# Optimization experiments

Hardware: AMD Instinct MI355X
Metric: run time of the kernel (lower is better)

Reference implementation:

```python
import jax, jax.numpy as jnp
import numpy as np

D_MODEL = 2048
N_HEADS = 16
D_HEAD = D_MODEL // N_HEADS
D_FF = 4 * D_MODEL
LN_EPS = 1e-5


def setup_inputs() -> dict:
    key = jax.random.key(0)
    ks = jax.random.split(key, 12)
    s = 1.0 / np.sqrt(D_MODEL)
    sf = 1.0 / np.sqrt(D_FF)
    return {
        "x": jax.random.normal(ks[0], (1, 2048, D_MODEL), dtype=jnp.float32),
        "ln1_g": jnp.ones((D_MODEL,), jnp.float32),
        "ln1_b": jnp.zeros((D_MODEL,), jnp.float32),
        # weights stored [in, out] (transpose of torch layout; equivalent under random init)
        "Wq": jax.random.normal(ks[1], (D_MODEL, D_MODEL), jnp.float32) * s,
        "Wk": jax.random.normal(ks[2], (D_MODEL, D_MODEL), jnp.float32) * s,
        "Wv": jax.random.normal(ks[3], (D_MODEL, D_MODEL), jnp.float32) * s,
        "Wp": jax.random.normal(ks[4], (D_MODEL, D_MODEL), jnp.float32) * s,
        "bp": jnp.zeros((D_MODEL,), jnp.float32),
        "ln2_g": jnp.ones((D_MODEL,), jnp.float32),
        "ln2_b": jnp.zeros((D_MODEL,), jnp.float32),
        "W1": jax.random.normal(ks[5], (D_MODEL, D_FF), jnp.float32) * s,
        "b1": jnp.zeros((D_FF,), jnp.float32),
        "W2": jax.random.normal(ks[6], (D_FF, D_MODEL), jnp.float32) * sf,
        "b2": jnp.zeros((D_MODEL,), jnp.float32),
    }


def _layer_norm(x, g, b):
    mu = jnp.mean(x, axis=-1, keepdims=True)
    var = jnp.mean(jnp.square(x - mu), axis=-1, keepdims=True)
    return (x - mu) * jax.lax.rsqrt(var + LN_EPS) * g + b


def _attention(h, Wq, Wk, Wv, Wp, bp):
    B, S, E = h.shape
    q = (h @ Wq).reshape(B, S, N_HEADS, D_HEAD)
    k = (h @ Wk).reshape(B, S, N_HEADS, D_HEAD)
    v = (h @ Wv).reshape(B, S, N_HEADS, D_HEAD)
    # [B, H, S, S] causal scores (matches the naive materialized original)
    scores = jnp.einsum("bqhd,bkhd->bhqk", q, k) / np.sqrt(D_HEAD).astype(np.float32)
    causal = jnp.arange(S)[:, None] >= jnp.arange(S)[None, :]
    scores = jnp.where(causal, scores, -jnp.inf)
    attn = jax.nn.softmax(scores, axis=-1)
    out = jnp.einsum("bhqk,bkhd->bqhd", attn, v).reshape(B, S, E)
    return out @ Wp + bp


def reference(x, ln1_g, ln1_b, Wq, Wk, Wv, Wp, bp, ln2_g, ln2_b, W1, b1, W2, b2):
    # attention branch: x += MHA(LN1(x)); dropout=0 (inference)
    x1 = x + _attention(_layer_norm(x, ln1_g, ln1_b), Wq, Wk, Wv, Wp, bp)
    # ff branch: FeedForward adds its own residual on the normalized input
    g = _layer_norm(x1, ln2_g, ln2_b)
    mlp = jax.nn.gelu(g @ W1 + b1, approximate=False) @ W2 + b2
    return x1 + (g + mlp)
```

## Files before the change

### kernel.cpp

```cpp
#include <hip/hip_runtime.h>
#include <math.h>

typedef unsigned int u32;
typedef unsigned short u16;
typedef __attribute__((ext_vector_type(8))) short short8;
typedef __attribute__((ext_vector_type(4))) float f32x4;

__device__ __forceinline__ u16 f2bf(float f) {
  u32 u = __builtin_bit_cast(u32, f);
  u += 0x7FFFu + ((u >> 16) & 1u);
  return (u16)(u >> 16);
}
__device__ __forceinline__ float bf2f(u16 h) {
  u32 u = ((u32)h) << 16;
  return __builtin_bit_cast(float, u);
}
__device__ __forceinline__ void gload_lds16(const void* g, void* l) {
  __builtin_amdgcn_global_load_lds((const __attribute__((address_space(1))) u32*)g,
                                   (__attribute__((address_space(3))) u32*)l, 16, 0, 0);
}
__device__ __forceinline__ f32x4 mfma16(short8 a, short8 b, f32x4 c) {
  return __builtin_amdgcn_mfma_f32_16x16x32_bf16(a, b, c, 0, 0, 0);
}

__global__ __launch_bounds__(256) void transpose_cast(const float* __restrict__ src,
                                                      u16* __restrict__ dst, int K, int N) {
  __shared__ __attribute__((aligned(16))) u16 tile[64][72];
  const int n0 = blockIdx.x * 64, k0 = blockIdx.y * 64;
  const int t = threadIdx.x;
  const int tr = t >> 4;
  const int tc4 = (t & 15) * 4;
#pragma unroll
  for (int p = 0; p < 4; ++p) {
    int row = p * 16 + tr;
    const float4 v = *(const float4*)(src + (size_t)(k0 + row) * N + n0 + tc4);
    tile[tc4 + 0][row] = f2bf(v.x);
    tile[tc4 + 1][row] = f2bf(v.y);
    tile[tc4 + 2][row] = f2bf(v.z);
    tile[tc4 + 3][row] = f2bf(v.w);
  }
  __syncthreads();
  const int nr = t >> 2;
  const int kc = (t & 3) * 16;
  u16* d = dst + (size_t)(n0 + nr) * K + k0 + kc;
  *(short8*)(d) = *(const short8*)&tile[nr][kc];
  *(short8*)(d + 8) = *(const short8*)&tile[nr][kc + 8];
}

__global__ __launch_bounds__(256) void transpose_v(const u16* __restrict__ qkv,
                                                   u16* __restrict__ vT) {
  __shared__ __attribute__((aligned(16))) u16 tile[64][72];
  const int kv0 = blockIdx.x * 64, d0 = blockIdx.y * 64, h = blockIdx.z;
  const int t = threadIdx.x;
  const int tr = t >> 3;
  const int tc8 = (t & 7) * 8;
#pragma unroll
  for (int p = 0; p < 2; ++p) {
    int row = p * 32 + tr;
    short8 v = *(const short8*)(qkv + (size_t)(kv0 + row) * 6144 + 4096 + h * 128 + d0 + tc8);
#pragma unroll
    for (int j = 0; j < 8; ++j) tile[tc8 + j][row] = (u16)v[j];
  }
  __syncthreads();
  const int dr = t >> 2;
  const int kc = (t & 3) * 16;
  u16* dst = vT + ((size_t)h * 128 + d0 + dr) * 2048 + kv0 + kc;
  *(short8*)dst = *(const short8*)&tile[dr][kc];
  *(short8*)(dst + 8) = *(const short8*)&tile[dr][kc + 8];
}

__global__ __launch_bounds__(256) void ln_kernel(const float* __restrict__ x,
                                                 const float* __restrict__ gw,
                                                 const float* __restrict__ bw,
                                                 u16* __restrict__ out) {
  const int row = blockIdx.x, t = threadIdx.x;
  const float* xr = x + (size_t)row * 2048;
  const float4 v0 = *(const float4*)(xr + t * 8);
  const float4 v1 = *(const float4*)(xr + t * 8 + 4);
  float s = v0.x + v0.y + v0.z + v0.w + v1.x + v1.y + v1.z + v1.w;
  float q = v0.x * v0.x + v0.y * v0.y + v0.z * v0.z + v0.w * v0.w +
            v1.x * v1.x + v1.y * v1.y + v1.z * v1.z + v1.w * v1.w;
#pragma unroll
  for (int w = 32; w; w >>= 1) { s += __shfl_xor(s, w); q += __shfl_xor(q, w); }
  __shared__ float rs[4], rq[4];
  const int wid = t >> 6, lane = t & 63;
  if (!lane) { rs[wid] = s; rq[wid] = q; }
  __syncthreads();
  s = rs[0] + rs[1] + rs[2] + rs[3];
  q = rq[0] + rq[1] + rq[2] + rq[3];
  const float mu = s * (1.f / 2048.f);
  const float var = q * (1.f / 2048.f) - mu * mu;
  const float rstd = rsqrtf(var + 1e-5f);
  const float4 g0 = *(const float4*)(gw + t * 8);
  const float4 g1 = *(const float4*)(gw + t * 8 + 4);
  const float4 b0 = *(const float4*)(bw + t * 8);
  const float4 b1 = *(const float4*)(bw + t * 8 + 4);
  short8 o;
  o[0] = (short)f2bf((v0.x - mu) * rstd * g0.x + b0.x);
  o[1] = (short)f2bf((v0.y - mu) * rstd * g0.y + b0.y);
  o[2] = (short)f2bf((v0.z - mu) * rstd * g0.z + b0.z);
  o[3] = (short)f2bf((v0.w - mu) * rstd * g0.w + b0.w);
  o[4] = (short)f2bf((v1.x - mu) * rstd * g1.x + b1.x);
  o[5] = (short)f2bf((v1.y - mu) * rstd * g1.y + b1.y);
  o[6] = (short)f2bf((v1.z - mu) * rstd * g1.z + b1.z);
  o[7] = (short)f2bf((v1.w - mu) * rstd * g1.w + b1.w);
  *(short8*)(out + (size_t)row * 2048 + t * 8) = o;
}

template <int EPI>
__global__ __launch_bounds__(512, 2) void gemm3(const u16* __restrict__ A,
                                                const u16* __restrict__ Bt,
                                                int M, int N, int K, int Kc,
                                                u16* __restrict__ outB,
                                                const float* __restrict__ bias,
                                                float* __restrict__ pA,
                                                float* __restrict__ pB) {
  __shared__ __attribute__((aligned(16))) u16 lds[3 * 16384];
  const int m0 = blockIdx.y * 256, n0 = blockIdx.x * 256;
  const int tid = threadIdx.x, wid = tid >> 6, lane = tid & 63;
  const int wr = wid >> 2, wc = wid & 3;
  const int lq = lane & 15, lk = lane >> 4;
  const int kStart = blockIdx.z * Kc;
  const int NT = Kc / 32;

  size_t aoff[2], boff[2];
#pragma unroll
  for (int s = 0; s < 2; ++s) {
    int c = s * 512 + tid;
    int row = c >> 2;
    int col = ((c & 3) ^ ((row >> 1) & 3)) * 8;
    aoff[s] = (size_t)(m0 + row) * K + kStart + col;
    boff[s] = (size_t)(n0 + row) * K + kStart + col;
  }
  u16* ldst = lds + tid * 8;

#define STA(s, buf, t2) gload_lds16(A + aoff[s] + (size_t)((t2) * 32), \
                                    ldst + (buf) * 16384 + (s) * 4096)
#define STB(s, buf, t2) gload_lds16(Bt + boff[s] + (size_t)((t2) * 32), \
                                    ldst + (buf) * 16384 + 8192 + (s) * 4096)

  STA(0, 0, 0); STA(1, 0, 0); STB(0, 0, 0); STB(1, 0, 0);
  STA(0, 1, 1); STA(1, 1, 1); STB(0, 1, 1); STB(1, 1, 1);
  asm volatile("s_waitcnt vmcnt(4)" ::: "memory");
  __builtin_amdgcn_s_barrier();
  __builtin_amdgcn_sched_barrier(0);

  f32x4 acc[8][4] = {};
  int cur = 0, nxt2 = 2;
  for (int t = 0; t < NT; ++t) {
    const char* bufc = (const char*)lds + cur * 32768;
    const bool st = (t + 2) < NT;
    short8 bf[4], af[4];
#pragma unroll
    for (int ni = 0; ni < 4; ++ni) {
      int br = wc * 64 + ni * 16 + lq;
      bf[ni] = *(const short8*)(bufc + 16384 + br * 64 + ((lk ^ ((br >> 1) & 3)) << 4));
    }
#pragma unroll
    for (int mi = 0; mi < 4; ++mi) {
      int ar = wr * 128 + mi * 16 + lq;
      af[mi] = *(const short8*)(bufc + ar * 64 + ((lk ^ ((ar >> 1) & 3)) << 4));
    }
    if (st) { STA(0, nxt2, t + 2); STA(1, nxt2, t + 2); }
    __builtin_amdgcn_s_setprio(1);
#pragma unroll
    for (int mi = 0; mi < 4; ++mi)
#pragma unroll
      for (int ni = 0; ni < 4; ++ni)
        acc[mi][ni] = mfma16(af[mi], bf[ni], acc[mi][ni]);
    __builtin_amdgcn_s_setprio(0);
#pragma unroll
    for (int mi = 0; mi < 4; ++mi) {
      int ar = wr * 128 + (mi + 4) * 16 + lq;
      af[mi] = *(const short8*)(bufc + ar * 64 + ((lk ^ ((ar >> 1) & 3)) << 4));
    }
    if (st) { STB(0, nxt2, t + 2); STB(1, nxt2, t + 2); }
    __builtin_amdgcn_s_setprio(1);
#pragma unroll
    for (int mi = 0; mi < 4; ++mi)
#pragma unroll
      for (int ni = 0; ni < 4; ++ni)
        acc[mi + 4][ni] = mfma16(af[mi], bf[ni], acc[mi + 4][ni]);
    __builtin_amdgcn_s_setprio(0);
    if (st) asm volatile("s_waitcnt vmcnt(4)" ::: "memory");
    else    asm volatile("s_waitcnt vmcnt(0)" ::: "memory");
    __builtin_amdgcn_s_barrier();
    __builtin_amdgcn_sched_barrier(0);
    cur = (cur == 2) ? 0 : cur + 1;
    nxt2 = (nxt2 == 2) ? 0 : nxt2 + 1;
  }
#undef STA
#undef STB

  float* pp = nullptr;
  if (EPI == 4) {
    pp = (blockIdx.z < 2 ? pA : pB) + (size_t)(blockIdx.z & 1) * ((size_t)M * N);
  }
#pragma unroll
  for (int mi = 0; mi < 8; ++mi) {
#pragma unroll
    for (int ni = 0; ni < 4; ++ni) {
      const int col = n0 + wc * 64 + ni * 16 + lq;
#pragma unroll
      for (int r = 0; r < 4; ++r) {
        const int row = m0 + wr * 128 + mi * 16 + lk * 4 + r;
        const size_t idx = (size_t)row * N + col;
        float v = acc[mi][ni][r];
        if (EPI == 0) {
          outB[idx] = f2bf(v);
        } else if (EPI == 2) {
          float xg = v + bias[col];
          outB[idx] = f2bf(0.5f * xg * (1.f + erff(xg * 0.70710678118654752f)));
        } else {
          pp[idx] = v;
        }
      }
    }
  }
}

template <int NS, int RES2>
__global__ __launch_bounds__(256) void reduce_kernel(const float* __restrict__ pA,
                                                     const float* __restrict__ pB,
                                                     const float* __restrict__ bias,
                                                     const float* __restrict__ res1,
                                                     const u16* __restrict__ res2,
                                                     float* __restrict__ out,
                                                     int MN, int N) {
  const int i = (blockIdx.x * 256 + threadIdx.x) * 4;
  if (i >= MN) return;
  float4 s = *(const float4*)(pA + i);
  {
    const float4 t = *(const float4*)(pA + MN + i);
    s.x += t.x; s.y += t.y; s.z += t.z; s.w += t.w;
  }
  if (NS == 4) {
    const float4 t0 = *(const float4*)(pB + i);
    const float4 t1 = *(const float4*)(pB + MN + i);
    s.x += t0.x + t1.x; s.y += t0.y + t1.y; s.z += t0.z + t1.z; s.w += t0.w + t1.w;
  }
  const int col = i & (N - 1);
  const float4 bv = *(const float4*)(bias + col);
  const float4 r1 = *(const float4*)(res1 + i);
  float4 o;
  o.x = s.x + bv.x + r1.x;
  o.y = s.y + bv.y + r1.y;
  o.z = s.z + bv.z + r1.z;
  o.w = s.w + bv.w + r1.w;
  if (RES2) {
    const u16* r2 = res2 + i;
    o.x += bf2f(r2[0]); o.y += bf2f(r2[1]); o.z += bf2f(r2[2]); o.w += bf2f(r2[3]);
  }
  *(float4*)(out + i) = o;
}

__global__ __launch_bounds__(256) void attn_kernel(const u16* __restrict__ qkv,
                                                   const u16* __restrict__ vT,
                                                   u16* __restrict__ attnout) {
  __shared__ __attribute__((aligned(16))) u16 lsK[64 * 128];
  __shared__ __attribute__((aligned(16))) u16 lsV[128 * 64];
  __shared__ __attribute__((aligned(16))) u16 lsP[4][16 * 64];
  const int h = blockIdx.x;
  const int qi = 31 - blockIdx.y;
  const int qb = qi * 64;
  const int tid = threadIdx.x, wid = tid >> 6, lane = tid & 63;
  const int lq = lane & 15, lk = lane >> 4;
  const int qw = qb + wid * 16;

  short8 qf[4];
  {
    const u16* qp = qkv + (size_t)(qw + lq) * 6144 + h * 128;
#pragma unroll
    for (int ks = 0; ks < 4; ++ks) qf[ks] = *(const short8*)(qp + ks * 32 + lk * 8);
  }
  float mreg[4], lreg[4];
  f32x4 o[8];
#pragma unroll
  for (int r = 0; r < 4; ++r) { mreg[r] = -INFINITY; lreg[r] = 0.f; }
#pragma unroll
  for (int dt = 0; dt < 8; ++dt) o[dt] = (f32x4){0.f, 0.f, 0.f, 0.f};

  const int rK = lane >> 4, sK = lane & 15;
  const int rV = lane >> 3, sV = lane & 7;
  const int nkt = qi + 1;
  for (int kt = 0; kt < nkt; ++kt) {
    const int kv0 = kt * 64;
    if (kt) __syncthreads();
#pragma unroll
    for (int i = 0; i < 4; ++i) {
      int c = wid * 4 + i;
      int rowK = c * 4 + rK;
      gload_lds16(qkv + (size_t)(kv0 + rowK) * 6144 + 2048 + h * 128 + ((sK ^ (rowK & 7)) * 8),
                  lsK + c * 512);
      int rowV = c * 8 + rV;
      gload_lds16(vT + ((size_t)h * 128 + rowV) * 2048 + kv0 + ((sV ^ (rowV & 7)) * 8),
                  lsV + c * 512);
    }
    __syncthreads();

    f32x4 sc[4];
#pragma unroll
    for (int nt = 0; nt < 4; ++nt) sc[nt] = (f32x4){0.f, 0.f, 0.f, 0.f};
#pragma unroll
    for (int ks = 0; ks < 4; ++ks) {
#pragma unroll
      for (int nt = 0; nt < 4; ++nt) {
        int kvr = nt * 16 + lq;
        short8 kf = *(const short8*)((const char*)lsK + kvr * 256 +
                                     ((ks * 64 + lk * 16) ^ ((kvr & 7) << 4)));
        sc[nt] = mfma16(qf[ks], kf, sc[nt]);
      }
    }
    float rmax[4] = {-INFINITY, -INFINITY, -INFINITY, -INFINITY};
#pragma unroll
    for (int nt = 0; nt < 4; ++nt) {
      int kv = kv0 + nt * 16 + lq;
#pragma unroll
      for (int r = 0; r < 4; ++r) {
        int qrow = qw + lk * 4 + r;
        float s = (kv <= qrow) ? sc[nt][r] * 0.08838834764831845f : -INFINITY;
        sc[nt][r] = s;
        rmax[r] = fmaxf(rmax[r], s);
      }
    }
#pragma unroll
    for (int r = 0; r < 4; ++r)
#pragma unroll
      for (int w = 1; w < 16; w <<= 1) rmax[r] = fmaxf(rmax[r], __shfl_xor(rmax[r], w));
    bool grow = false;
#pragma unroll
    for (int r = 0; r < 4; ++r) grow |= (rmax[r] > mreg[r] + 8.f);
    if (__any(grow)) {
#pragma unroll
      for (int r = 0; r < 4; ++r) {
        float mn = fmaxf(mreg[r], rmax[r]);
        float alpha = __expf(mreg[r] - mn);
        mreg[r] = mn;
        lreg[r] *= alpha;
#pragma unroll
        for (int dt = 0; dt < 8; ++dt) o[dt][r] *= alpha;
      }
    }
    float rsum[4] = {0.f, 0.f, 0.f, 0.f};
    u16* P = &lsP[wid][0];
#pragma unroll
    for (int nt = 0; nt < 4; ++nt) {
#pragma unroll
      for (int r = 0; r < 4; ++r) {
        float p = __expf(sc[nt][r] - mreg[r]);
        rsum[r] += p;
        int prow = lk * 4 + r, pcol = nt * 16 + lq;
        *(u16*)((char*)P + prow * 128 + ((pcol * 2) ^ ((prow & 7) << 4))) = f2bf(p);
      }
    }
#pragma unroll
    for (int r = 0; r < 4; ++r) {
#pragma unroll
      for (int w = 1; w < 16; w <<= 1) rsum[r] += __shfl_xor(rsum[r], w);
      lreg[r] += rsum[r];
    }
#pragma unroll
    for (int kk = 0; kk < 2; ++kk) {
      short8 pa = *(const short8*)((const char*)P + lq * 128 +
                                   ((kk * 64 + lk * 16) ^ ((lq & 7) << 4)));
#pragma unroll
      for (int dt = 0; dt < 8; ++dt) {
        int dr = dt * 16 + lq;
        short8 vf = *(const short8*)((const char*)lsV + dr * 128 +
                                     ((kk * 64 + lk * 16) ^ ((dr & 7) << 4)));
        o[dt] = mfma16(pa, vf, o[dt]);
      }
    }
  }
#pragma unroll
  for (int r = 0; r < 4; ++r) {
    float inv = 1.f / lreg[r];
    int row = qw + lk * 4 + r;
    u16* op = attnout + (size_t)row * 2048 + h * 128 + lq;
#pragma unroll
    for (int dt = 0; dt < 8; ++dt) op[dt * 16] = f2bf(o[dt][r] * inv);
  }
}

extern "C" void kernel_launch(void* const* d_in, const int* in_sizes, int n_in,
                              void* d_out, int out_size, void* d_ws, size_t ws_size,
                              hipStream_t stream) {
  (void)in_sizes; (void)n_in; (void)out_size; (void)ws_size;
  const float* x    = (const float*)d_in[0];
  const float* ln1g = (const float*)d_in[1];
  const float* ln1b = (const float*)d_in[2];
  const float* Wq   = (const float*)d_in[3];
  const float* Wk   = (const float*)d_in[4];
  const float* Wv   = (const float*)d_in[5];
  const float* Wp   = (const float*)d_in[6];
  const float* bp   = (const float*)d_in[7];
  const float* ln2g = (const float*)d_in[8];
  const float* ln2b = (const float*)d_in[9];
  const float* W1   = (const float*)d_in[10];
  const float* b1   = (const float*)d_in[11];
  const float* W2   = (const float*)d_in[12];
  const float* b2   = (const float*)d_in[13];
  float* out = (float*)d_out;
  char* ws = (char*)d_ws;

  u16* wqkvT = (u16*)(ws + 0);
  u16* hbuf  = (u16*)(ws + 25165824);
  u16* wpT   = (u16*)(ws + 33554432);
  u16* w1T   = (u16*)(ws + 41943040);
  u16* w2T   = (u16*)(ws + 75497472);
  u16* qkv   = (u16*)(ws + 109051904);
  u16* vT    = (u16*)(ws + 134217728);
  u16* attn  = (u16*)(ws + 142606336);
  float* x1  = (float*)(ws + 150994944);
  u16* g     = (u16*)(ws + 167772160);
  u16* ff1   = (u16*)(ws + 0);
  float* projPA = (float*)(ws + 0);
  float* projPB = (float*)(ws + 109051904);
  float* ffPA = (float*)(ws + 33554432);
  float* ffPB = (float*)(ws + 109051904);

  dim3 b256(256), b512(512);
  transpose_cast<<<dim3(32, 32), b256, 0, stream>>>(Wq, wqkvT, 2048, 2048);
  transpose_cast<<<dim3(32, 32), b256, 0, stream>>>(Wk, wqkvT + 2048 * 2048, 2048, 2048);
  transpose_cast<<<dim3(32, 32), b256, 0, stream>>>(Wv, wqkvT + 4096 * 2048, 2048, 2048);
  transpose_cast<<<dim3(32, 32), b256, 0, stream>>>(Wp, wpT, 2048, 2048);
  transpose_cast<<<dim3(128, 32), b256, 0, stream>>>(W1, w1T, 2048, 8192);
  transpose_cast<<<dim3(32, 128), b256, 0, stream>>>(W2, w2T, 8192, 2048);
  ln_kernel<<<2048, b256, 0, stream>>>(x, ln1g, ln1b, hbuf);
  gemm3<0><<<dim3(24, 8, 1), b512, 0, stream>>>(hbuf, wqkvT, 2048, 6144, 2048, 2048,
                                                qkv, nullptr, nullptr, nullptr);
  transpose_v<<<dim3(32, 2, 16), b256, 0, stream>>>(qkv, vT);
  attn_kernel<<<dim3(16, 32), b256, 0, stream>>>(qkv, vT, attn);
  gemm3<4><<<dim3(8, 8, 4), b512, 0, stream>>>(attn, wpT, 2048, 2048, 2048, 512,
                                               nullptr, nullptr, projPA, projPB);
  reduce_kernel<4, 0><<<4096, b256, 0, stream>>>(projPA, projPB, bp, x, nullptr, x1,
                                                 4194304, 2048);
  ln_kernel<<<2048, b256, 0, stream>>>(x1, ln2g, ln2b, g);
  gemm3<2><<<dim3(32, 8, 1), b512, 0, stream>>>(g, w1T, 2048, 8192, 2048, 2048,
                                                ff1, b1, nullptr, nullptr);
  gemm3<4><<<dim3(8, 8, 4), b512, 0, stream>>>(ff1, w2T, 2048, 2048, 8192, 2048,
                                               nullptr, nullptr, ffPA, ffPB);
  reduce_kernel<4, 1><<<4096, b256, 0, stream>>>(ffPA, ffPB, b2, x1, g, out,
                                                 4194304, 2048);
}
```

Before: 423.8 us.

## Rewrite GEMM mainloop with 64-wide K tiles and 8-phase ping-pong pipeline

Replaces the GEMM main loop's 3-buffer, 32-wide-K pipeline with two 64-wide-K LDS buffers (128 KB total) and a new XOR swizzle. Each pair of K tiles is split into eight phases that interleave LDS fragment reads, staged global-to-LDS loads of A and B halves, and MFMA bursts, with barriers between phases. Launch bounds drop to one block per CU to fit the larger LDS footprint. The aim is to hide global load latency and cut per-iteration barrier and wait overhead. The cost is lower occupancy and more barriers per K step.

New measurement: 590.3 us. 39.3% more time.

```diff
diff --git a/kernel.cpp b/kernel.cpp
--- a/kernel.cpp
+++ b/kernel.cpp
@@ -108,89 +108,107 @@
 }
 
 template <int EPI>
-__global__ __launch_bounds__(512, 2) void gemm3(const u16* __restrict__ A,
+__global__ __launch_bounds__(512, 1) void gemm4(const u16* __restrict__ A,
                                                 const u16* __restrict__ Bt,
                                                 int M, int N, int K, int Kc,
                                                 u16* __restrict__ outB,
                                                 const float* __restrict__ bias,
                                                 float* __restrict__ pA,
                                                 float* __restrict__ pB) {
-  __shared__ __attribute__((aligned(16))) u16 lds[3 * 16384];
+  __shared__ __attribute__((aligned(16))) u16 lds[65536];
   const int m0 = blockIdx.y * 256, n0 = blockIdx.x * 256;
   const int tid = threadIdx.x, wid = tid >> 6, lane = tid & 63;
   const int wr = wid >> 2, wc = wid & 3;
   const int lq = lane & 15, lk = lane >> 4;
+  const int xorq = (lq & 7) << 4;
   const int kStart = blockIdx.z * Kc;
-  const int NT = Kc / 32;
-
-  size_t aoff[2], boff[2];
-#pragma unroll
-  for (int s = 0; s < 2; ++s) {
-    int c = s * 512 + tid;
-    int row = c >> 2;
-    int col = ((c & 3) ^ ((row >> 1) & 3)) * 8;
-    aoff[s] = (size_t)(m0 + row) * K + kStart + col;
-    boff[s] = (size_t)(n0 + row) * K + kStart + col;
-  }
-  u16* ldst = lds + tid * 8;
-
-#define STA(s, buf, t2) gload_lds16(A + aoff[s] + (size_t)((t2) * 32), \
-                                    ldst + (buf) * 16384 + (s) * 4096)
-#define STB(s, buf, t2) gload_lds16(Bt + boff[s] + (size_t)((t2) * 32), \
-                                    ldst + (buf) * 16384 + 8192 + (s) * 4096)
-
-  STA(0, 0, 0); STA(1, 0, 0); STB(0, 0, 0); STB(1, 0, 0);
-  STA(0, 1, 1); STA(1, 1, 1); STB(0, 1, 1); STB(1, 1, 1);
-  asm volatile("s_waitcnt vmcnt(4)" ::: "memory");
+  const int NT = Kc / 64;
+  const char* ldsB = (const char*)lds;
+
+  const int srow = lane >> 3;
+  const int scol = ((lane & 7) ^ srow) * 8;
+  size_t aSrc[2][2], bSrc[2][2];
+#pragma unroll
+  for (int h = 0; h < 2; ++h)
+#pragma unroll
+    for (int s = 0; s < 2; ++s) {
+      int r = h * 128 + (s * 8 + wid) * 8 + srow;
+      aSrc[h][s] = (size_t)(m0 + r) * K + kStart + scol;
+      bSrc[h][s] = (size_t)(n0 + r) * K + kStart + scol;
+    }
+
+#define STG_A(P, h, s, kt) gload_lds16(A + aSrc[h][s] + (size_t)(kt) * 64, \
+    lds + (P) * 32768 + (h) * 8192 + ((s) * 8 + wid) * 512 + lane * 8)
+#define STG_B(P, h, s, kt) gload_lds16(Bt + bSrc[h][s] + (size_t)(kt) * 64, \
+    lds + (P) * 32768 + 16384 + (h) * 8192 + ((s) * 8 + wid) * 512 + lane * 8)
+#define RD_A(P, mi, ks) (*(const short8*)(ldsB + (P) * 65536 + \
+    (wr * 128 + (mi) * 16 + lq) * 128 + (((ks) * 64 + lk * 16) ^ xorq)))
+#define RD_B(P, ni, ks) (*(const short8*)(ldsB + (P) * 65536 + 32768 + \
+    (wc * 64 + (ni) * 16 + lq) * 128 + (((ks) * 64 + lk * 16) ^ xorq)))
+
+  STG_A(0, 0, 0, 0); STG_A(0, 0, 1, 0); STG_A(0, 1, 0, 0); STG_A(0, 1, 1, 0);
+  STG_B(0, 0, 0, 0); STG_B(0, 0, 1, 0); STG_B(0, 1, 0, 0); STG_B(0, 1, 1, 0);
+  STG_A(1, 0, 0, 1); STG_A(1, 0, 1, 1); STG_A(1, 1, 0, 1); STG_A(1, 1, 1, 1);
+  STG_B(1, 0, 0, 1); STG_B(1, 0, 1, 1); STG_B(1, 1, 0, 1); STG_B(1, 1, 1, 1);
+  asm volatile("s_waitcnt vmcnt(8)" ::: "memory");
   __builtin_amdgcn_s_barrier();
   __builtin_amdgcn_sched_barrier(0);
 
   f32x4 acc[8][4] = {};
-  int cur = 0, nxt2 = 2;
-  for (int t = 0; t < NT; ++t) {
-    const char* bufc = (const char*)lds + cur * 32768;
-    const bool st = (t + 2) < NT;
-    short8 bf[4], af[4];
-#pragma unroll
-    for (int ni = 0; ni < 4; ++ni) {
-      int br = wc * 64 + ni * 16 + lq;
-      bf[ni] = *(const short8*)(bufc + 16384 + br * 64 + ((lk ^ ((br >> 1) & 3)) << 4));
-    }
-#pragma unroll
-    for (int mi = 0; mi < 4; ++mi) {
-      int ar = wr * 128 + mi * 16 + lq;
-      af[mi] = *(const short8*)(bufc + ar * 64 + ((lk ^ ((ar >> 1) & 3)) << 4));
-    }
-    if (st) { STA(0, nxt2, t + 2); STA(1, nxt2, t + 2); }
-    __builtin_amdgcn_s_setprio(1);
-#pragma unroll
-    for (int mi = 0; mi < 4; ++mi)
-#pragma unroll
-      for (int ni = 0; ni < 4; ++ni)
-        acc[mi][ni] = mfma16(af[mi], bf[ni], acc[mi][ni]);
-    __builtin_amdgcn_s_setprio(0);
-#pragma unroll
-    for (int mi = 0; mi < 4; ++mi) {
-      int ar = wr * 128 + (mi + 4) * 16 + lq;
-      af[mi] = *(const short8*)(bufc + ar * 64 + ((lk ^ ((ar >> 1) & 3)) << 4));
-    }
-    if (st) { STB(0, nxt2, t + 2); STB(1, nxt2, t + 2); }
-    __builtin_amdgcn_s_setprio(1);
-#pragma unroll
-    for (int mi = 0; mi < 4; ++mi)
-#pragma unroll
-      for (int ni = 0; ni < 4; ++ni)
-        acc[mi + 4][ni] = mfma16(af[mi], bf[ni], acc[mi + 4][ni]);
-    __builtin_amdgcn_s_setprio(0);
-    if (st) asm volatile("s_waitcnt vmcnt(4)" ::: "memory");
-    else    asm volatile("s_waitcnt vmcnt(0)" ::: "memory");
-    __builtin_amdgcn_s_barrier();
-    __builtin_amdgcn_sched_barrier(0);
-    cur = (cur == 2) ? 0 : cur + 1;
-    nxt2 = (nxt2 == 2) ? 0 : nxt2 + 1;
-  }
-#undef STA
-#undef STB
+
+#define PH(P, ks, HI, RDB, STAGES, WAITS) { \
+    short8 a_[4]; \
+    if (RDB) { \
+      bfr[0] = RD_B(P, 0, ks); bfr[1] = RD_B(P, 1, ks); \
+      bfr[2] = RD_B(P, 2, ks); bfr[3] = RD_B(P, 3, ks); \
+    } \
+    a_[0] = RD_A(P, (HI) * 4 + 0, ks); a_[1] = RD_A(P, (HI) * 4 + 1, ks); \
+    a_[2] = RD_A(P, (HI) * 4 + 2, ks); a_[3] = RD_A(P, (HI) * 4 + 3, ks); \
+    STAGES \
+    __builtin_amdgcn_s_barrier(); \
+    asm volatile("s_waitcnt lgkmcnt(0)" ::: "memory"); \
+    __builtin_amdgcn_sched_barrier(0); \
+    __builtin_amdgcn_s_setprio(1); \
+    _Pragma("unroll") \
+    for (int mi_ = 0; mi_ < 4; ++mi_) { \
+      _Pragma("unroll") \
+      for (int ni_ = 0; ni_ < 4; ++ni_) \
+        acc[(HI) * 4 + mi_][ni_] = mfma16(a_[mi_], bfr[ni_], acc[(HI) * 4 + mi_][ni_]); \
+    } \
+    __builtin_amdgcn_s_setprio(0); \
+    WAITS \
+    __builtin_amdgcn_s_barrier(); \
+    __builtin_amdgcn_sched_barrier(0); \
+  }
+
+  for (int I = 0; I < NT / 2; ++I) {
+    const int t = 2 * I, u = t + 1;
+    const bool sAu = I > 0;
+    const bool sT2 = (t + 2) < NT;
+    const bool sU2 = (u + 2) < NT;
+    short8 bfr[4];
+    PH(0, 0, 0, 1, { if (sAu) { STG_A(1, 0, 0, u); STG_A(1, 0, 1, u); } }, {})
+    PH(0, 0, 1, 0, { if (sAu) { STG_A(1, 1, 0, u); STG_A(1, 1, 1, u); } }, {})
+    PH(0, 1, 0, 1, {}, {})
+    PH(0, 1, 1, 0,
+       { if (sT2) { STG_B(0, 0, 0, t + 2); STG_B(0, 0, 1, t + 2);
+                    STG_B(0, 1, 0, t + 2); STG_B(0, 1, 1, t + 2); } },
+       { if (sT2) { asm volatile("s_waitcnt vmcnt(4)" ::: "memory"); }
+         else     { asm volatile("s_waitcnt vmcnt(0)" ::: "memory"); } })
+    PH(1, 0, 0, 1, { if (sT2) { STG_A(0, 0, 0, t + 2); STG_A(0, 0, 1, t + 2); } }, {})
+    PH(1, 0, 1, 0, { if (sT2) { STG_A(0, 1, 0, t + 2); STG_A(0, 1, 1, t + 2); } }, {})
+    PH(1, 1, 0, 1, {}, {})
+    PH(1, 1, 1, 0,
+       { if (sU2) { STG_B(1, 0, 0, u + 2); STG_B(1, 0, 1, u + 2);
+                    STG_B(1, 1, 0, u + 2); STG_B(1, 1, 1, u + 2); } },
+       { if (sU2) { asm volatile("s_waitcnt vmcnt(4)" ::: "memory"); }
+         else     { asm volatile("s_waitcnt vmcnt(0)" ::: "memory"); } })
+  }
+#undef PH
+#undef STG_A
+#undef STG_B
+#undef RD_A
+#undef RD_B
 
   float* pp = nullptr;
   if (EPI == 4) {
@@ -427,18 +445,18 @@
   transpose_cast<<<dim3(128, 32), b256, 0, stream>>>(W1, w1T, 2048, 8192);
   transpose_cast<<<dim3(32, 128), b256, 0, stream>>>(W2, w2T, 8192, 2048);
   ln_kernel<<<2048, b256, 0, stream>>>(x, ln1g, ln1b, hbuf);
-  gemm3<0><<<dim3(24, 8, 1), b512, 0, stream>>>(hbuf, wqkvT, 2048, 6144, 2048, 2048,
+  gemm4<0><<<dim3(24, 8, 1), b512, 0, stream>>>(hbuf, wqkvT, 2048, 6144, 2048, 2048,
                                                 qkv, nullptr, nullptr, nullptr);
   transpose_v<<<dim3(32, 2, 16), b256, 0, stream>>>(qkv, vT);
   attn_kernel<<<dim3(16, 32), b256, 0, stream>>>(qkv, vT, attn);
-  gemm3<4><<<dim3(8, 8, 4), b512, 0, stream>>>(attn, wpT, 2048, 2048, 2048, 512,
+  gemm4<4><<<dim3(8, 8, 4), b512, 0, stream>>>(attn, wpT, 2048, 2048, 2048, 512,
                                                nullptr, nullptr, projPA, projPB);
   reduce_kernel<4, 0><<<4096, b256, 0, stream>>>(projPA, projPB, bp, x, nullptr, x1,
                                                  4194304, 2048);
   ln_kernel<<<2048, b256, 0, stream>>>(x1, ln2g, ln2b, g);
-  gemm3<2><<<dim3(32, 8, 1), b512, 0, stream>>>(g, w1T, 2048, 8192, 2048, 2048,
+  gemm4<2><<<dim3(32, 8, 1), b512, 0, stream>>>(g, w1T, 2048, 8192, 2048, 2048,
                                                 ff1, b1, nullptr, nullptr);
-  gemm3<4><<<dim3(8, 8, 4), b512, 0, stream>>>(ff1, w2T, 2048, 2048, 8192, 2048,
+  gemm4<4><<<dim3(8, 8, 4), b512, 0, stream>>>(ff1, w2T, 2048, 2048, 8192, 2048,
                                                nullptr, nullptr, ffPA, ffPB);
   reduce_kernel<4, 1><<<4096, b256, 0, stream>>>(ffPA, ffPB, b2, x1, g, out,
                                                  4194304, 2048);
```
